# Kernel tuning notes

Hardware: AMD Instinct MI355X
Metric: run time of the kernel (lower is better)

The kernel has to match this reference:

```python
import jax, jax.numpy as jnp
import numpy as np

B, P, S, D, H = 4, 8, 2048, 1024, 16
DEPTH = D // H
WINDOW = 64
TIMESTEP = 1024  # static decode step index, > WINDOW to exercise sliding-window branch


def _split_heads(x):
    # (B,P,S,D) -> (B,P,H,S,depth)
    b, p = x.shape[0], x.shape[1]
    return x.reshape(b, p, -1, H, DEPTH).transpose(0, 1, 3, 2, 4)


def _concat_heads(x):
    # (B,P,H,S,depth) -> (B,P,S,D)
    b, p = x.shape[0], x.shape[1]
    return x.transpose(0, 1, 3, 2, 4).reshape(b, p, -1, D)


def setup_inputs() -> dict:
    key = jax.random.key(0)
    ks = jax.random.split(key, 11)
    w_scale = 1.0 / np.sqrt(D).astype(np.float32)
    return {
        "inputs": jax.random.normal(ks[0], (B, P, 1, D), jnp.float32),
        "K": jax.random.normal(ks[1], (B, P, S, D), jnp.float32),
        "V": jax.random.normal(ks[2], (B, P, S, D), jnp.float32),
        "Wq": jax.random.normal(ks[3], (D, D), jnp.float32) * w_scale,
        "bq": jnp.zeros((D,), jnp.float32),
        "Wk": jax.random.normal(ks[4], (D, D), jnp.float32) * w_scale,
        "bk": jnp.zeros((D,), jnp.float32),
        "Wv": jax.random.normal(ks[5], (D, D), jnp.float32) * w_scale,
        "bv": jnp.zeros((D,), jnp.float32),
        "Wo": jax.random.normal(ks[6], (D, D), jnp.float32) * w_scale,
        "bo": jnp.zeros((D,), jnp.float32),
        "timestep": TIMESTEP,
    }


def reference(inputs, K, V, Wq, bq, Wk, bk, Wv, bv, Wo, bo, timestep):
    # projections on the single decode token (noise disabled, as in default Layer)
    q = _split_heads(inputs @ Wq + bq)  # (B,P,H,1,depth)
    k = _split_heads(inputs @ Wk + bk)
    v = _split_heads(inputs @ Wv + bv)
    Kh = _split_heads(K)  # (B,P,H,S,depth)
    Vh = _split_heads(V)
    # cache update: concat(K[:t], k, K[t+1:]) == write k at position t
    Kh = Kh.at[:, :, :, timestep:timestep + 1, :].set(k)
    Vh = Vh.at[:, :, :, timestep:timestep + 1, :].set(v)
    # full-length scores, scaled by sqrt(depth) (dk = last dim of K)
    logits = jnp.einsum('bphqd,bphsd->bphqs', q, Kh) / jnp.sqrt(
        jnp.asarray(DEPTH, jnp.float32))  # (B,P,H,1,S)
    lo = timestep - WINDOW if (WINDOW is not None and timestep > WINDOW) else 0
    pos = jnp.arange(S)
    valid = (pos >= lo) & (pos <= timestep)  # sliding window [t-w, t]
    logits = jnp.where(valid, logits, jnp.asarray(-1e9, logits.dtype))
    attn = jax.nn.softmax(logits, axis=-1)  # (B,P,H,1,S)
    z = jnp.einsum('bphqs,bphsd->bphqd', attn, Vh)  # (B,P,H,1,depth)
    z = _concat_heads(z) @ Wo + bo  # (B,P,1,D)
    return z, _concat_heads(Kh), _concat_heads(Vh), attn
```

## Files before the change

kernel.cpp:

```cpp
#include <hip/hip_runtime.h>

#define SS 2048
#define DD 1024
#define HH 16
#define DEPTH 64
#define WINDOW 64
#define NTOK 32
#define KV_ELEMS (NTOK*SS*DD)
#define N4 (KV_ELEMS/4)
#define TOT4 (2*N4)

#define WS_Q 0
#define WS_K (NTOK*DD)
#define WS_V (2*NTOK*DD)
#define WS_Z (3*NTOK*DD)

typedef float f4 __attribute__((ext_vector_type(4)));

__device__ __forceinline__ void copy_kv(const float* __restrict__ K,
                                        const float* __restrict__ V,
                                        float* __restrict__ outK,
                                        float* __restrict__ outV,
                                        int t, int start, int end,
                                        int cbid, int ncblk) {
    const f4* __restrict__ K4 = (const f4*)K;
    const f4* __restrict__ V4 = (const f4*)V;
    f4* __restrict__ oK4 = (f4*)outK;
    f4* __restrict__ oV4 = (f4*)outV;
    const int stride = ncblk * blockDim.x;
    for (int i = start + cbid * blockDim.x + (int)threadIdx.x; i < end; i += stride) {
        if (i < N4) {
            if (((i >> 8) & (SS - 1)) == t) continue;
            f4 val = __builtin_nontemporal_load(K4 + i);
            __builtin_nontemporal_store(val, oK4 + i);
        } else {
            const int j = i - N4;
            if (((j >> 8) & (SS - 1)) == t) continue;
            f4 val = __builtin_nontemporal_load(V4 + j);
            __builtin_nontemporal_store(val, oV4 + j);
        }
    }
}

#define NPROJ 48
#define K1COPY 1600

__global__ __launch_bounds__(512)
void k1_proj_copy(const float* __restrict__ x,
                  const float* __restrict__ K, const float* __restrict__ V,
                  const float* __restrict__ Wq, const float* __restrict__ bq,
                  const float* __restrict__ Wk, const float* __restrict__ bk,
                  const float* __restrict__ Wv, const float* __restrict__ bv,
                  const int* __restrict__ tptr,
                  float* __restrict__ ws,
                  float* __restrict__ outK, float* __restrict__ outV,
                  int c0, int c1) {
    const int t = *tptr;
    if (blockIdx.x >= NPROJ) {
        copy_kv(K, V, outK, outV, t, c0, c1, blockIdx.x - NPROJ, gridDim.x - NPROJ);
        return;
    }
    __shared__ __align__(16) float xs[NTOK][128];
    const int m     = blockIdx.x >> 4;
    const int chunk = blockIdx.x & 15;
    const float* __restrict__ W  = (m == 0) ? Wq : (m == 1) ? Wk : Wv;
    const float* __restrict__ bb = (m == 0) ? bq : (m == 1) ? bk : bv;
    const int lane = threadIdx.x & 63;
    const int tg   = threadIdx.x >> 6;
    const int j    = chunk * 64 + lane;
    const int tok0 = tg * 4;

    float acc0, acc1, acc2, acc3;
    acc0 = acc1 = acc2 = acc3 = bb[j];

    for (int c = 0; c < 8; ++c) {
        __syncthreads();
        for (int r = threadIdx.x; r < NTOK * 32; r += 512) {
            const int tok = r >> 5, q4 = r & 31;
            ((f4*)xs[tok])[q4] = ((const f4*)(x + (size_t)tok * DD + c * 128))[q4];
        }
        __syncthreads();
        const float* Wc = W + (size_t)(c * 128) * DD + j;
        #pragma unroll 2
        for (int il4 = 0; il4 < 32; ++il4) {
            const int il = il4 * 4;
            const float w0 = Wc[(size_t)(il + 0) * DD];
            const float w1 = Wc[(size_t)(il + 1) * DD];
            const float w2 = Wc[(size_t)(il + 2) * DD];
            const float w3 = Wc[(size_t)(il + 3) * DD];
            const f4 x0 = ((const f4*)xs[tok0 + 0])[il4];
            const f4 x1 = ((const f4*)xs[tok0 + 1])[il4];
            const f4 x2 = ((const f4*)xs[tok0 + 2])[il4];
            const f4 x3 = ((const f4*)xs[tok0 + 3])[il4];
            acc0 = fmaf(w3, x0.w, fmaf(w2, x0.z, fmaf(w1, x0.y, fmaf(w0, x0.x, acc0))));
            acc1 = fmaf(w3, x1.w, fmaf(w2, x1.z, fmaf(w1, x1.y, fmaf(w0, x1.x, acc1))));
            acc2 = fmaf(w3, x2.w, fmaf(w2, x2.z, fmaf(w1, x2.y, fmaf(w0, x2.x, acc2))));
            acc3 = fmaf(w3, x3.w, fmaf(w2, x3.z, fmaf(w1, x3.y, fmaf(w0, x3.x, acc3))));
        }
    }
    float* dst = ws + m * (NTOK * DD);
    dst[(size_t)(tok0 + 0) * DD + j] = acc0;
    dst[(size_t)(tok0 + 1) * DD + j] = acc1;
    dst[(size_t)(tok0 + 2) * DD + j] = acc2;
    dst[(size_t)(tok0 + 3) * DD + j] = acc3;
    if (m == 1) {
        outK[((size_t)(tok0 + 0) * SS + t) * DD + j] = acc0;
        outK[((size_t)(tok0 + 1) * SS + t) * DD + j] = acc1;
        outK[((size_t)(tok0 + 2) * SS + t) * DD + j] = acc2;
        outK[((size_t)(tok0 + 3) * SS + t) * DD + j] = acc3;
    } else if (m == 2) {
        outV[((size_t)(tok0 + 0) * SS + t) * DD + j] = acc0;
        outV[((size_t)(tok0 + 1) * SS + t) * DD + j] = acc1;
        outV[((size_t)(tok0 + 2) * SS + t) * DD + j] = acc2;
        outV[((size_t)(tok0 + 3) * SS + t) * DD + j] = acc3;
    }
}

#define NATTN 128
#define K2COPY 1024

__global__ __launch_bounds__(256)
void k2_attn_copy(const float* __restrict__ K, const float* __restrict__ V,
                  const int* __restrict__ tptr,
                  float* __restrict__ ws, float* __restrict__ outA,
                  float* __restrict__ outK, float* __restrict__ outV,
                  int c0, int c1) {
    const int t = *tptr;
    if (blockIdx.x >= NATTN) {
        copy_kv(K, V, outK, outV, t, c0, c1, blockIdx.x - NATTN, gridDim.x - NATTN);
        return;
    }
    const int wv   = threadIdx.x >> 6;
    const int lane = threadIdx.x & 63;
    const int tok  = blockIdx.x >> 2;
    const int h0   = (blockIdx.x & 3) * 4;
    const int h    = h0 + wv;

    __shared__ float qh[4][DEPTH], kh[4][DEPTH], vh[4][DEPTH];
    __shared__ float sc[4][WINDOW + 8];

    {
        const int base = tok * DD + h0 * DEPTH;
        ((float*)qh)[threadIdx.x] = ws[WS_Q + base + threadIdx.x];
        ((float*)kh)[threadIdx.x] = ws[WS_K + base + threadIdx.x];
        ((float*)vh)[threadIdx.x] = ws[WS_V + base + threadIdx.x];
    }
    __syncthreads();

    const int lo    = (t > WINDOW) ? (t - WINDOW) : 0;
    const int count = t - lo + 1;
    const size_t kvbase = (size_t)tok * SS * DD + h * DEPTH;

    for (int jj = lane; jj < count; jj += 64) {
        const int s = lo + jj;
        float acc = 0.f;
        if (s == t) {
            #pragma unroll
            for (int d = 0; d < DEPTH; ++d) acc = fmaf(qh[wv][d], kh[wv][d], acc);
        } else {
            const f4* kr = (const f4*)(K + kvbase + (size_t)s * DD);
            #pragma unroll
            for (int d4 = 0; d4 < DEPTH / 4; ++d4) {
                const f4 kk = kr[d4];
                acc = fmaf(qh[wv][d4 * 4 + 0], kk.x, acc);
                acc = fmaf(qh[wv][d4 * 4 + 1], kk.y, acc);
                acc = fmaf(qh[wv][d4 * 4 + 2], kk.z, acc);
                acc = fmaf(qh[wv][d4 * 4 + 3], kk.w, acc);
            }
        }
        sc[wv][jj] = acc * 0.125f;
    }

    float mx = -1e30f;
    for (int jj = lane; jj < count; jj += 64) mx = fmaxf(mx, sc[wv][jj]);
    #pragma unroll
    for (int o = 32; o; o >>= 1) mx = fmaxf(mx, __shfl_xor(mx, o));
    float sum = 0.f;
    for (int jj = lane; jj < count; jj += 64) {
        const float e = expf(sc[wv][jj] - mx);
        sc[wv][jj] = e;
        sum += e;
    }
    #pragma unroll
    for (int o = 32; o; o >>= 1) sum += __shfl_xor(sum, o);
    const float inv = 1.f / sum;
    for (int jj = lane; jj < count; jj += 64) sc[wv][jj] *= inv;

    {
        f4* oa = (f4*)(outA + ((size_t)tok * HH + h) * SS);
        for (int q4 = lane; q4 < SS / 4; q4 += 64) {
            const int s0 = q4 * 4;
            f4 val;
            val.x = (s0 + 0 >= lo && s0 + 0 <= t) ? sc[wv][s0 + 0 - lo] : 0.f;
            val.y = (s0 + 1 >= lo && s0 + 1 <= t) ? sc[wv][s0 + 1 - lo] : 0.f;
            val.z = (s0 + 2 >= lo && s0 + 2 <= t) ? sc[wv][s0 + 2 - lo] : 0.f;
            val.w = (s0 + 3 >= lo && s0 + 3 <= t) ? sc[wv][s0 + 3 - lo] : 0.f;
            __builtin_nontemporal_store(val, oa + q4);
        }
    }

    {
        float acc = 0.f;
        #pragma unroll 4
        for (int jj = 0; jj < count - 1; ++jj)
            acc = fmaf(sc[wv][jj], V[kvbase + (size_t)(lo + jj) * DD + lane], acc);
        acc = fmaf(sc[wv][count - 1], vh[wv][lane], acc);
        ws[WS_Z + (size_t)tok * DD + h * DEPTH + lane] = acc;
    }
}

#define NOUT 16
#define K3COPY 768

__global__ __launch_bounds__(512)
void k3_out_copy(const float* __restrict__ K, const float* __restrict__ V,
                 const float* __restrict__ Wo, const float* __restrict__ bo,
                 const int* __restrict__ tptr,
                 const float* __restrict__ ws,
                 float* __restrict__ outZ,
                 float* __restrict__ outK, float* __restrict__ outV,
                 int c0, int c1) {
    const int t = *tptr;
    if (blockIdx.x >= NOUT) {
        copy_kv(K, V, outK, outV, t, c0, c1, blockIdx.x - NOUT, gridDim.x - NOUT);
        return;
    }
    __shared__ __align__(16) float zsh[NTOK][128];
    const int chunk = blockIdx.x;
    const int lane = threadIdx.x & 63;
    const int tg   = threadIdx.x >> 6;
    const int j    = chunk * 64 + lane;
    const int tok0 = tg * 4;
    const float* __restrict__ z = ws + WS_Z;

    float acc0, acc1, acc2, acc3;
    acc0 = acc1 = acc2 = acc3 = bo[j];

    for (int c = 0; c < 8; ++c) {
        __syncthreads();
        for (int r = threadIdx.x; r < NTOK * 32; r += 512) {
            const int tok = r >> 5, q4 = r & 31;
            ((f4*)zsh[tok])[q4] = ((const f4*)(z + (size_t)tok * DD + c * 128))[q4];
        }
        __syncthreads();
        const float* Wc = Wo + (size_t)(c * 128) * DD + j;
        #pragma unroll 2
        for (int il4 = 0; il4 < 32; ++il4) {
            const int il = il4 * 4;
            const float w0 = Wc[(size_t)(il + 0) * DD];
            const float w1 = Wc[(size_t)(il + 1) * DD];
            const float w2 = Wc[(size_t)(il + 2) * DD];
            const float w3 = Wc[(size_t)(il + 3) * DD];
            const f4 x0 = ((const f4*)zsh[tok0 + 0])[il4];
            const f4 x1 = ((const f4*)zsh[tok0 + 1])[il4];
            const f4 x2 = ((const f4*)zsh[tok0 + 2])[il4];
            const f4 x3 = ((const f4*)zsh[tok0 + 3])[il4];
            acc0 = fmaf(w3, x0.w, fmaf(w2, x0.z, fmaf(w1, x0.y, fmaf(w0, x0.x, acc0))));
            acc1 = fmaf(w3, x1.w, fmaf(w2, x1.z, fmaf(w1, x1.y, fmaf(w0, x1.x, acc1))));
            acc2 = fmaf(w3, x2.w, fmaf(w2, x2.z, fmaf(w1, x2.y, fmaf(w0, x2.x, acc2))));
            acc3 = fmaf(w3, x3.w, fmaf(w2, x3.z, fmaf(w1, x3.y, fmaf(w0, x3.x, acc3))));
        }
    }
    outZ[(size_t)(tok0 + 0) * DD + j] = acc0;
    outZ[(size_t)(tok0 + 1) * DD + j] = acc1;
    outZ[(size_t)(tok0 + 2) * DD + j] = acc2;
    outZ[(size_t)(tok0 + 3) * DD + j] = acc3;
}

extern "C" void kernel_launch(void* const* d_in, const int* in_sizes, int n_in,
                              void* d_out, int out_size, void* d_ws, size_t ws_size,
                              hipStream_t stream) {
    const float* x  = (const float*)d_in[0];
    const float* K  = (const float*)d_in[1];
    const float* V  = (const float*)d_in[2];
    const float* Wq = (const float*)d_in[3];
    const float* bq = (const float*)d_in[4];
    const float* Wk = (const float*)d_in[5];
    const float* bk = (const float*)d_in[6];
    const float* Wv = (const float*)d_in[7];
    const float* bv = (const float*)d_in[8];
    const float* Wo = (const float*)d_in[9];
    const float* bo = (const float*)d_in[10];
    const int* tptr = (const int*)d_in[11];

    float* out  = (float*)d_out;
    float* outZ = out;
    float* outK = out + 32768;
    float* outV = outK + KV_ELEMS;
    float* outA = outV + KV_ELEMS;
    float* ws   = (float*)d_ws;

    const int C2 = 10485760;

    k1_proj_copy<<<NPROJ + K1COPY, 512, 0, stream>>>(
        x, K, V, Wq, bq, Wk, bk, Wv, bv, tptr, ws, outK, outV, 0, N4);
    k2_attn_copy<<<NATTN + K2COPY, 256, 0, stream>>>(
        K, V, tptr, ws, outA, outK, outV, N4, N4 + C2);
    k3_out_copy<<<NOUT + K3COPY, 512, 0, stream>>>(
        K, V, Wo, bo, tptr, ws, outZ, outK, outV, N4 + C2, TOT4);
}
```

Baseline: 258.3 us.

## Fuse attention with output projection and split K/V copies across two kernels

Merges the attention kernel and the output projection into one kernel with one 1024-thread block per token. Each block computes all heads, keeps z in shared memory and applies Wo directly, which removes the third launch and the workspace round trip for z. The cache copy is reorganised so kernel 1 copies all of K and kernel 2 copies all of V. Each copy thread issues four independent loads per sweep over a fixed stride and skips the slot at position t. The trade-off is a serial 1024-step dot product per thread for the output projection, with Wo re-read by each of the 32 token blocks, and copy work that is no longer balanced against the compute blocks.

```diff
diff --git a/kernel.cpp b/kernel.cpp
--- a/kernel.cpp
+++ b/kernel.cpp
@@ -8,7 +8,7 @@
 #define NTOK 32
 #define KV_ELEMS (NTOK*SS*DD)
 #define N4 (KV_ELEMS/4)
-#define TOT4 (2*N4)
+#define CPT 524288
 
 #define WS_Q 0
 #define WS_K (NTOK*DD)
@@ -17,47 +17,42 @@
 
 typedef float f4 __attribute__((ext_vector_type(4)));
 
-__device__ __forceinline__ void copy_kv(const float* __restrict__ K,
-                                        const float* __restrict__ V,
-                                        float* __restrict__ outK,
-                                        float* __restrict__ outV,
-                                        int t, int start, int end,
-                                        int cbid, int ncblk) {
-    const f4* __restrict__ K4 = (const f4*)K;
-    const f4* __restrict__ V4 = (const f4*)V;
-    f4* __restrict__ oK4 = (f4*)outK;
-    f4* __restrict__ oV4 = (f4*)outV;
-    const int stride = ncblk * blockDim.x;
-    for (int i = start + cbid * blockDim.x + (int)threadIdx.x; i < end; i += stride) {
-        if (i < N4) {
-            if (((i >> 8) & (SS - 1)) == t) continue;
-            f4 val = __builtin_nontemporal_load(K4 + i);
-            __builtin_nontemporal_store(val, oK4 + i);
-        } else {
-            const int j = i - N4;
-            if (((j >> 8) & (SS - 1)) == t) continue;
-            f4 val = __builtin_nontemporal_load(V4 + j);
-            __builtin_nontemporal_store(val, oV4 + j);
-        }
+__device__ __forceinline__ void copy_tensor(const float* __restrict__ src,
+                                            float* __restrict__ dst,
+                                            int t, int lin) {
+    const f4* __restrict__ s4 = (const f4*)src;
+    f4* __restrict__ d4 = (f4*)dst;
+    int i = lin;
+    #pragma unroll
+    for (int sweep = 0; sweep < 8; ++sweep) {
+        const int i0 = i, i1 = i + CPT, i2 = i + 2 * CPT, i3 = i + 3 * CPT;
+        const f4 v0 = s4[i0];
+        const f4 v1 = s4[i1];
+        const f4 v2 = s4[i2];
+        const f4 v3 = s4[i3];
+        if (((i0 >> 8) & (SS - 1)) != t) __builtin_nontemporal_store(v0, d4 + i0);
+        if (((i1 >> 8) & (SS - 1)) != t) __builtin_nontemporal_store(v1, d4 + i1);
+        if (((i2 >> 8) & (SS - 1)) != t) __builtin_nontemporal_store(v2, d4 + i2);
+        if (((i3 >> 8) & (SS - 1)) != t) __builtin_nontemporal_store(v3, d4 + i3);
+        i += 4 * CPT;
     }
 }
 
 #define NPROJ 48
-#define K1COPY 1600
+#define K1CB  1024
 
 __global__ __launch_bounds__(512)
-void k1_proj_copy(const float* __restrict__ x,
-                  const float* __restrict__ K, const float* __restrict__ V,
-                  const float* __restrict__ Wq, const float* __restrict__ bq,
-                  const float* __restrict__ Wk, const float* __restrict__ bk,
-                  const float* __restrict__ Wv, const float* __restrict__ bv,
-                  const int* __restrict__ tptr,
-                  float* __restrict__ ws,
-                  float* __restrict__ outK, float* __restrict__ outV,
-                  int c0, int c1) {
+void k1_proj_copyK(const float* __restrict__ x,
+                   const float* __restrict__ K,
+                   const float* __restrict__ Wq, const float* __restrict__ bq,
+                   const float* __restrict__ Wk, const float* __restrict__ bk,
+                   const float* __restrict__ Wv, const float* __restrict__ bv,
+                   const int* __restrict__ tptr,
+                   float* __restrict__ ws,
+                   float* __restrict__ outK, float* __restrict__ outV) {
     const int t = *tptr;
     if (blockIdx.x >= NPROJ) {
-        copy_kv(K, V, outK, outV, t, c0, c1, blockIdx.x - NPROJ, gridDim.x - NPROJ);
+        copy_tensor(K, outK, t, (blockIdx.x - NPROJ) * 512 + (int)threadIdx.x);
         return;
     }
     __shared__ __align__(16) float xs[NTOK][128];
@@ -95,6 +90,7 @@
             acc0 = fmaf(w3, x0.w, fmaf(w2, x0.z, fmaf(w1, x0.y, fmaf(w0, x0.x, acc0))));
             acc1 = fmaf(w3, x1.w, fmaf(w2, x1.z, fmaf(w1, x1.y, fmaf(w0, x1.x, acc1))));
             acc2 = fmaf(w3, x2.w, fmaf(w2, x2.z, fmaf(w1, x2.y, fmaf(w0, x2.x, acc2))));
+            ac3:
             acc3 = fmaf(w3, x3.w, fmaf(w2, x3.z, fmaf(w1, x3.y, fmaf(w0, x3.x, acc3))));
         }
     }
@@ -116,56 +112,54 @@
     }
 }
 
-#define NATTN 128
-#define K2COPY 1024
-
-__global__ __launch_bounds__(256)
-void k2_attn_copy(const float* __restrict__ K, const float* __restrict__ V,
-                  const int* __restrict__ tptr,
-                  float* __restrict__ ws, float* __restrict__ outA,
-                  float* __restrict__ outK, float* __restrict__ outV,
-                  int c0, int c1) {
+#define K2CB 512
+
+__global__ __launch_bounds__(1024)
+void k2_attn_out_copyV(const float* __restrict__ K, const float* __restrict__ V,
+                       const float* __restrict__ Wo, const float* __restrict__ bo,
+                       const int* __restrict__ tptr,
+                       float* __restrict__ ws,
+                       float* __restrict__ outZ, float* __restrict__ outA,
+                       float* __restrict__ outV) {
     const int t = *tptr;
-    if (blockIdx.x >= NATTN) {
-        copy_kv(K, V, outK, outV, t, c0, c1, blockIdx.x - NATTN, gridDim.x - NATTN);
+    if (blockIdx.x >= NTOK) {
+        copy_tensor(V, outV, t, (blockIdx.x - NTOK) * 1024 + (int)threadIdx.x);
         return;
     }
-    const int wv   = threadIdx.x >> 6;
-    const int lane = threadIdx.x & 63;
-    const int tok  = blockIdx.x >> 2;
-    const int h0   = (blockIdx.x & 3) * 4;
-    const int h    = h0 + wv;
-
-    __shared__ float qh[4][DEPTH], kh[4][DEPTH], vh[4][DEPTH];
-    __shared__ float sc[4][WINDOW + 8];
-
-    {
-        const int base = tok * DD + h0 * DEPTH;
-        ((float*)qh)[threadIdx.x] = ws[WS_Q + base + threadIdx.x];
-        ((float*)kh)[threadIdx.x] = ws[WS_K + base + threadIdx.x];
-        ((float*)vh)[threadIdx.x] = ws[WS_V + base + threadIdx.x];
-    }
+    const int tok  = blockIdx.x;
+    const int tid  = threadIdx.x;
+    const int wv   = tid >> 6;
+    const int lane = tid & 63;
+
+    __shared__ float qs[DD], ks[DD], vs[DD], zs[DD];
+    __shared__ float sc[HH][WINDOW + 8];
+
+    qs[tid] = ws[WS_Q + (size_t)tok * DD + tid];
+    ks[tid] = ws[WS_K + (size_t)tok * DD + tid];
+    vs[tid] = ws[WS_V + (size_t)tok * DD + tid];
     __syncthreads();
 
     const int lo    = (t > WINDOW) ? (t - WINDOW) : 0;
     const int count = t - lo + 1;
-    const size_t kvbase = (size_t)tok * SS * DD + h * DEPTH;
+    const size_t kvbase = (size_t)tok * SS * DD + wv * DEPTH;
+    const int hbase = wv * DEPTH;
 
     for (int jj = lane; jj < count; jj += 64) {
         const int s = lo + jj;
         float acc = 0.f;
         if (s == t) {
             #pragma unroll
-            for (int d = 0; d < DEPTH; ++d) acc = fmaf(qh[wv][d], kh[wv][d], acc);
+            for (int d = 0; d < DEPTH; ++d)
+                acc = fmaf(qs[hbase + d], ks[hbase + d], acc);
         } else {
             const f4* kr = (const f4*)(K + kvbase + (size_t)s * DD);
             #pragma unroll
             for (int d4 = 0; d4 < DEPTH / 4; ++d4) {
                 const f4 kk = kr[d4];
-                acc = fmaf(qh[wv][d4 * 4 + 0], kk.x, acc);
-                acc = fmaf(qh[wv][d4 * 4 + 1], kk.y, acc);
-                acc = fmaf(qh[wv][d4 * 4 + 2], kk.z, acc);
-                acc = fmaf(qh[wv][d4 * 4 + 3], kk.w, acc);
+                acc = fmaf(qs[hbase + d4 * 4 + 0], kk.x, acc);
+                acc = fmaf(qs[hbase + d4 * 4 + 1], kk.y, acc);
+                acc = fmaf(qs[hbase + d4 * 4 + 2], kk.z, acc);
+                acc = fmaf(qs[hbase + d4 * 4 + 3], kk.w, acc);
             }
         }
         sc[wv][jj] = acc * 0.125f;
@@ -187,7 +181,7 @@
     for (int jj = lane; jj < count; jj += 64) sc[wv][jj] *= inv;
 
     {
-        f4* oa = (f4*)(outA + ((size_t)tok * HH + h) * SS);
+        f4* oa = (f4*)(outA + ((size_t)tok * HH + wv) * SS);
         for (int q4 = lane; q4 < SS / 4; q4 += 64) {
             const int s0 = q4 * 4;
             f4 val;
@@ -204,67 +198,18 @@
         #pragma unroll 4
         for (int jj = 0; jj < count - 1; ++jj)
             acc = fmaf(sc[wv][jj], V[kvbase + (size_t)(lo + jj) * DD + lane], acc);
-        acc = fmaf(sc[wv][count - 1], vh[wv][lane], acc);
-        ws[WS_Z + (size_t)tok * DD + h * DEPTH + lane] = acc;
-    }
-}
-
-#define NOUT 16
-#define K3COPY 768
-
-__global__ __launch_bounds__(512)
-void k3_out_copy(const float* __restrict__ K, const float* __restrict__ V,
-                 const float* __restrict__ Wo, const float* __restrict__ bo,
-                 const int* __restrict__ tptr,
-                 const float* __restrict__ ws,
-                 float* __restrict__ outZ,
-                 float* __restrict__ outK, float* __restrict__ outV,
-                 int c0, int c1) {
-    const int t = *tptr;
-    if (blockIdx.x >= NOUT) {
-        copy_kv(K, V, outK, outV, t, c0, c1, blockIdx.x - NOUT, gridDim.x - NOUT);
-        return;
-    }
-    __shared__ __align__(16) float zsh[NTOK][128];
-    const int chunk = blockIdx.x;
-    const int lane = threadIdx.x & 63;
-    const int tg   = threadIdx.x >> 6;
-    const int j    = chunk * 64 + lane;
-    const int tok0 = tg * 4;
-    const float* __restrict__ z = ws + WS_Z;
-
-    float acc0, acc1, acc2, acc3;
-    acc0 = acc1 = acc2 = acc3 = bo[j];
-
-    for (int c = 0; c < 8; ++c) {
-        __syncthreads();
-        for (int r = threadIdx.x; r < NTOK * 32; r += 512) {
-            const int tok = r >> 5, q4 = r & 31;
-            ((f4*)zsh[tok])[q4] = ((const f4*)(z + (size_t)tok * DD + c * 128))[q4];
-        }
-        __syncthreads();
-        const float* Wc = Wo + (size_t)(c * 128) * DD + j;
-        #pragma unroll 2
-        for (int il4 = 0; il4 < 32; ++il4) {
-            const int il = il4 * 4;
-            const float w0 = Wc[(size_t)(il + 0) * DD];
-            const float w1 = Wc[(size_t)(il + 1) * DD];
-            const float w2 = Wc[(size_t)(il + 2) * DD];
-            const float w3 = Wc[(size_t)(il + 3) * DD];
-            const f4 x0 = ((const f4*)zsh[tok0 + 0])[il4];
-            const f4 x1 = ((const f4*)zsh[tok0 + 1])[il4];
-            const f4 x2 = ((const f4*)zsh[tok0 + 2])[il4];
-            const f4 x3 = ((const f4*)zsh[tok0 + 3])[il4];
-            acc0 = fmaf(w3, x0.w, fmaf(w2, x0.z, fmaf(w1, x0.y, fmaf(w0, x0.x, acc0))));
-            acc1 = fmaf(w3, x1.w, fmaf(w2, x1.z, fmaf(w1, x1.y, fmaf(w0, x1.x, acc1))));
-            acc2 = fmaf(w3, x2.w, fmaf(w2, x2.z, fmaf(w1, x2.y, fmaf(w0, x2.x, acc2))));
-            acc3 = fmaf(w3, x3.w, fmaf(w2, x3.z, fmaf(w1, x3.y, fmaf(w0, x3.x, acc3))));
-        }
-    }
-    outZ[(size_t)(tok0 + 0) * DD + j] = acc0;
-    outZ[(size_t)(tok0 + 1) * DD + j] = acc1;
-    outZ[(size_t)(tok0 + 2) * DD + j] = acc2;
-    outZ[(size_t)(tok0 + 3) * DD + j] = acc3;
+        acc = fmaf(sc[wv][count - 1], vs[hbase + lane], acc);
+        zs[hbase + lane] = acc;
+    }
+    __syncthreads();
+
+    {
+        float ao = bo[tid];
+        #pragma unroll 8
+        for (int i2 = 0; i2 < DD; ++i2)
+            ao = fmaf(zs[i2], Wo[(size_t)i2 * DD + tid], ao);
+        outZ[(size_t)tok * DD + tid] = ao;
+    }
 }
 
 extern "C" void kernel_launch(void* const* d_in, const int* in_sizes, int n_in,
@@ -290,12 +235,8 @@
     float* outA = outV + KV_ELEMS;
     float* ws   = (float*)d_ws;
 
-    const int C2 = 10485760;
-
-    k1_proj_copy<<<NPROJ + K1COPY, 512, 0, stream>>>(
-        x, K, V, Wq, bq, Wk, bk, Wv, bv, tptr, ws, outK, outV, 0, N4);
-    k2_attn_copy<<<NATTN + K2COPY, 256, 0, stream>>>(
-        K, V, tptr, ws, outA, outK, outV, N4, N4 + C2);
-    k3_out_copy<<<NOUT + K3COPY, 512, 0, stream>>>(
-        K, V, Wo, bo, tptr, ws, outZ, outK, outV, N4 + C2, TOT4);
-}
+    k1_proj_copyK<<<NPROJ + K1CB, 512, 0, stream>>>(
+        x, K, Wq, bq, Wk, bk, Wv, bv, tptr, ws, outK, outV);
+    k2_attn_out_copyV<<<NTOK + K2CB, 1024, 0, stream>>>(
+        K, V, Wo, bo, tptr, ws, outZ, outA, outV);
+}
```

Result: slower. 323.6 us (+25.3%).
